# Kernel optimization log

Hardware: AMD Instinct MI355X
Metric: run time of the kernel (lower is better)

The kernel has to match this reference:

```python
import jax, jax.numpy as jnp
import numpy as np

DIM = 1024
NUM_HEADS = 16
HEAD_DIM = DIM // NUM_HEADS
EPS = 1e-5


def setup_inputs() -> dict:
    key = jax.random.key(0)
    ks = jax.random.split(key, 5)
    B, N = 2, 2048
    x = jax.random.normal(ks[0], (B, N, DIM), dtype=jnp.float32)
    # nn.Linear(dim, 3*dim): weight [3*dim, dim], bias [3*dim]
    w_qkv = jax.random.normal(ks[1], (3 * DIM, DIM), dtype=jnp.float32) * (DIM ** -0.5)
    b_qkv = jnp.zeros((3 * DIM,), dtype=jnp.float32)
    # qk-norm LayerNorm(head_dim) affine params
    q_gamma = jnp.ones((HEAD_DIM,), dtype=jnp.float32)
    q_beta = jnp.zeros((HEAD_DIM,), dtype=jnp.float32)
    k_gamma = jnp.ones((HEAD_DIM,), dtype=jnp.float32)
    k_beta = jnp.zeros((HEAD_DIM,), dtype=jnp.float32)
    # output projection nn.Linear(dim, dim)
    w_proj = jax.random.normal(ks[2], (DIM, DIM), dtype=jnp.float32) * (DIM ** -0.5)
    b_proj = jnp.zeros((DIM,), dtype=jnp.float32)
    return {
        "x": x,
        "w_qkv": w_qkv, "b_qkv": b_qkv,
        "q_gamma": q_gamma, "q_beta": q_beta,
        "k_gamma": k_gamma, "k_beta": k_beta,
        "w_proj": w_proj, "b_proj": b_proj,
    }


def _layernorm(t, gamma, beta):
    # LayerNorm over last dim (head_dim)
    mu = jnp.mean(t, axis=-1, keepdims=True)
    var = jnp.mean(jnp.square(t - mu), axis=-1, keepdims=True)
    return (t - mu) * jax.lax.rsqrt(var + EPS) * gamma + beta


def reference(x, w_qkv, b_qkv, q_gamma, q_beta, k_gamma, k_beta, w_proj, b_proj):
    B, N, C = x.shape
    H, D = NUM_HEADS, HEAD_DIM
    scale = D ** -0.5
    # QKV projection: [B,N,3C] -> [3,B,H,N,D]
    qkv = x @ w_qkv.T + b_qkv
    qkv = qkv.reshape(B, N, 3, H, D).transpose(2, 0, 3, 1, 4)
    q, k, v = qkv[0], qkv[1], qkv[2]
    # per-head qk-norm
    q = _layernorm(q, q_gamma, q_beta)
    k = _layernorm(k, k_gamma, k_beta)
    # scaled dot-product attention
    scores = jnp.einsum("bhqd,bhkd->bhqk", q, k) * scale
    attn = jax.nn.softmax(scores, axis=-1)
    out = jnp.einsum("bhqk,bhkd->bhqd", attn, v)  # [B,H,N,D]
    out = out.transpose(0, 2, 1, 3).reshape(B, N, C)
    # output projection
    return out @ w_proj.T + b_proj
```

## Files before the change

kernel.cpp:

```cpp
#include <hip/hip_runtime.h>

typedef _Float16 half8 __attribute__((ext_vector_type(8)));
typedef _Float16 half4 __attribute__((ext_vector_type(4)));
typedef float f32x4 __attribute__((ext_vector_type(4)));
typedef float f32x16 __attribute__((ext_vector_type(16)));
typedef unsigned int uint;
typedef uint uint2v __attribute__((ext_vector_type(2)));
typedef uint uint4v __attribute__((ext_vector_type(4)));

#define MFMA16(a, b, c) __builtin_amdgcn_mfma_f32_16x16x32_f16((a), (b), (c), 0, 0, 0)
#define MFMA32(a, b, c) __builtin_amdgcn_mfma_f32_32x32x16_f16((a), (b), (c), 0, 0, 0)

#define GLOAD16(g, l)                                            \
    __builtin_amdgcn_global_load_lds(                            \
        (const __attribute__((address_space(1))) void*)(g),      \
        (__attribute__((address_space(3))) void*)(l), 16, 0, 0)


__global__ __launch_bounds__(256) void cvt_all(const float* __restrict__ x,
                                               const float* __restrict__ wq,
                                               const float* __restrict__ wp,
                                               _Float16* __restrict__ xh,
                                               _Float16* __restrict__ wqh,
                                               _Float16* __restrict__ wph) {
    int i = blockIdx.x * 256 + threadIdx.x;
    const float* src;
    _Float16* dst;
    int off;
    if (i < 524288) { src = x; dst = xh; off = i; }
    else if (i < 917504) { src = wq; dst = wqh; off = i - 524288; }
    else { src = wp; dst = wph; off = i - 917504; }
    const float4* p = reinterpret_cast<const float4*>(src) + 2 * (size_t)off;
    float4 a = p[0], b = p[1];
    half8 o;
    o[0] = (_Float16)a.x; o[1] = (_Float16)a.y; o[2] = (_Float16)a.z; o[3] = (_Float16)a.w;
    o[4] = (_Float16)b.x; o[5] = (_Float16)b.y; o[6] = (_Float16)b.z; o[7] = (_Float16)b.w;
    reinterpret_cast<half8*>(dst)[off] = o;
}

template <int MT, int NT, int EPI>
__global__ __launch_bounds__(256) void gemm_nt(const _Float16* __restrict__ A,
                                               const _Float16* __restrict__ W,
                                               const float* __restrict__ bias,
                                               void* __restrict__ Cout, int K,
                                               const float* __restrict__ qg,
                                               const float* __restrict__ qb,
                                               const float* __restrict__ kg,
                                               const float* __restrict__ kb) {
    constexpr int TM = MT * 32;
    constexpr int TN = NT * 32;
    __shared__ __align__(16) _Float16 Al[2][TM * 64];
    __shared__ __align__(16) _Float16 Wl[2][TN * 64];
    const int tid = threadIdx.x, l = tid & 63, w = tid >> 6;
    const int lin = blockIdx.x + (blockIdx.y << 6);
    const int nwg = gridDim.x * gridDim.y;
    const int wg = (lin & 7) * (nwg >> 3) + (lin >> 3);
    const int bm = (wg & 63) * TM, bn = (wg >> 6) * TN;
    const int wr = (w >> 1) * (MT * 16), wc = (w & 1) * (NT * 16);
    const int srow = l >> 3;
    const int schunk = (l & 7) ^ srow;

    const _Float16* Ag = A + (size_t)(bm + (TM / 4) * w + srow) * K + 8 * schunk;
    const _Float16* Wg = W + (size_t)(bn + (TN / 4) * w + srow) * K + 8 * schunk;
    const int rswz = (l & 7) << 3;
    const int nk = K >> 6;

    auto stage = [&](int t, int buf) {
        const int kt = t << 6;
#pragma unroll
        for (int i = 0; i < MT; i++)
            GLOAD16(Ag + (size_t)(8 * i) * K + kt, &Al[buf][((TM / 4) * w + 8 * i) * 64]);
#pragma unroll
        for (int i = 0; i < NT; i++)
            GLOAD16(Wg + (size_t)(8 * i) * K + kt, &Wl[buf][((TN / 4) * w + 8 * i) * 64]);
    };

    f32x4 acc[MT][NT] = {};
    stage(0, 0);
    __syncthreads();
    for (int t = 0; t < nk; ++t) {
        const int cur = t & 1;
        if (t + 1 < nk) stage(t + 1, cur ^ 1);
#pragma unroll
        for (int ks = 0; ks < 2; ks++) {
            const int koff = (ks * 32 + (l >> 4) * 8) ^ rswz;
            half8 af[MT], wf[NT];
#pragma unroll
            for (int i = 0; i < MT; i++)
                af[i] = *(const half8*)&Al[cur][(wr + i * 16 + (l & 15)) * 64 + koff];
#pragma unroll
            for (int i = 0; i < NT; i++)
                wf[i] = *(const half8*)&Wl[cur][(wc + i * 16 + (l & 15)) * 64 + koff];
            __builtin_amdgcn_s_setprio(1);
#pragma unroll
            for (int mt = 0; mt < MT; mt++)
#pragma unroll
                for (int nt = 0; nt < NT; nt++)
                    acc[mt][nt] = MFMA16(af[mt], wf[nt], acc[mt][nt]);
            __builtin_amdgcn_s_setprio(0);
        }
        __syncthreads();
    }

    if (EPI == 0) {
        const int ncol = bn + wc;
        const int s = ncol >> 10;
        const int hh = (ncol >> 6) & 15;
        const float* gam = (s == 0) ? qg : kg;
        const float* bet = (s == 0) ? qb : kb;
        float ga[4], be[4];
        if (s < 2) {
#pragma unroll
            for (int nt = 0; nt < 4; nt++) {
                int d = nt * 16 + (l & 15);
                ga[nt] = gam[d];
                be[nt] = bet[d];
            }
        }
        const float cs = (s == 0) ? 0.18033688f : 1.f;
#pragma unroll
        for (int mt = 0; mt < MT; mt++)
#pragma unroll
            for (int r = 0; r < 4; r++) {
                float v[4];
                float sm = 0.f, s2 = 0.f;
#pragma unroll
                for (int nt = 0; nt < 4; nt++) {
                    v[nt] = acc[mt][nt][r] + bias[ncol + nt * 16 + (l & 15)];
                    sm += v[nt];
                    s2 += v[nt] * v[nt];
                }
                int m = bm + wr + mt * 16 + (l >> 4) * 4 + r;
                int b = m >> 11, nn = m & 2047;
                _Float16* dst = (_Float16*)Cout +
                    (size_t)((((s * 2 + b) * 16 + hh) * 2048 + nn) << 6);
                if (s < 2) {
#pragma unroll
                    for (int off = 1; off < 16; off <<= 1) {
                        sm += __shfl_xor(sm, off);
                        s2 += __shfl_xor(s2, off);
                    }
                    float mean = sm * (1.f / 64.f);
                    float var = s2 * (1.f / 64.f) - mean * mean;
                    float rs = rsqrtf(var + 1e-5f) * cs;
#pragma unroll
                    for (int nt = 0; nt < 4; nt++) {
                        int d = nt * 16 + (l & 15);
                        dst[d] = (_Float16)((v[nt] - mean) * rs * ga[nt] + be[nt] * cs);
                    }
                } else {
#pragma unroll
                    for (int nt = 0; nt < 4; nt++)
                        dst[nt * 16 + (l & 15)] = (_Float16)v[nt];
                }
            }
    } else {
#pragma unroll
        for (int mt = 0; mt < MT; mt++)
#pragma unroll
            for (int nt = 0; nt < NT; nt++)
#pragma unroll
                for (int r = 0; r < 4; r++) {
                    int m = bm + wr + mt * 16 + (l >> 4) * 4 + r;
                    int n = bn + wc + nt * 16 + (l & 15);
                    ((float*)Cout)[(size_t)m * 1024 + n] = acc[mt][nt][r] + bias[n];
                }
    }
}

template <int SPLIT>
__global__ __launch_bounds__(256, 4) void attn_kernel(const _Float16* __restrict__ qkv,
                                                      _Float16* __restrict__ out,
                                                      float* __restrict__ lpart) {
    const int tid = threadIdx.x;
    const int l = tid & 63, w = tid >> 6;
    const int l31 = l & 31, hi = l >> 5;
    const int bid = blockIdx.x;
    const int nwg = 512 * SPLIT;
    const int wg = (bid & 7) * (nwg >> 3) + (bid >> 3);
    int head, qt, quarter;
    if (SPLIT == 4) { head = wg >> 6; qt = (wg >> 2) & 15; quarter = wg & 3; }
    else            { head = wg >> 4; qt = wg & 15;        quarter = 0; }
    const int b = head >> 4, h = head & 15;
    const size_t hstride = (size_t)2048 * 64;
    const _Float16* Q = qkv + (size_t)((0 + b) * 16 + h) * hstride;
    const _Float16* Kp = qkv + (size_t)((2 + b) * 16 + h) * hstride + (size_t)quarter * 512 * 64;
    const _Float16* Vp = qkv + (size_t)((4 + b) * 16 + h) * hstride + (size_t)quarter * 512 * 64;
    const int NIT = (SPLIT == 4) ? 8 : 32;

    __shared__ __align__(16) _Float16 Kl[2][64 * 64];
    __shared__ __align__(16) _Float16 Vt[2][64 * 64];

    const int r0q = qt * 128 + w * 32;
    half8 qf[4];
    {
        const _Float16* Qrow = Q + (size_t)(r0q + l31) * 64 + 8 * hi;
#pragma unroll
        for (int dk = 0; dk < 4; dk++) qf[dk] = *(const half8*)&Qrow[16 * dk];
    }

    const int srow = l >> 3, sch = l & 7;
    auto stageK = [&](int it, _Float16* dst) {
#pragma unroll
        for (int t = 0; t < 2; t++) {
            int r0 = 16 * w + 8 * t;
            const _Float16* g = Kp + (size_t)(it * 64 + r0 + srow) * 64 + 8 * (sch ^ srow);
            GLOAD16(g, &dst[r0 * 64]);
        }
    };
    auto loadV = [&](int it, half8& v0, half8& v1) {
        const _Float16* g = Vp + (size_t)(it * 64 + 16 * w + srow) * 64 + 8 * sch;
        v0 = *(const half8*)g;
        v1 = *(const half8*)(g + 8 * 64);
    };
    auto scatterV = [&](half8 v0, half8 v1, _Float16* dst) {
        const int j0 = 16 * w + srow;
        const int d0 = 8 * sch;
#pragma unroll
        for (int i = 0; i < 8; i++) {
            const int sw = (i ^ sch) << 3;
            dst[(d0 + i) * 64 + (j0 ^ sw)] = v0[i];
            dst[(d0 + i) * 64 + ((j0 + 8) ^ sw)] = v1[i];
        }
    };

    float lrun = 0.f;
    f32x16 o0 = {}, o1 = {};

    half8 va, vb;
    stageK(0, Kl[0]);
    loadV(0, va, vb);
    scatterV(va, vb, Vt[0]);
    __syncthreads();

    const int kswz = (l31 & 7) << 3;
    const int vswz0 = ((l31 & 7) ^ (l31 >> 3)) << 3;
    const int vswz1 = vswz0 ^ (4 << 3);

    for (int it = 0; it < NIT; ++it) {
        const int cur = it & 1;
        const _Float16* Kc = Kl[cur];
        const _Float16* Vc = Vt[cur];
        if (it + 1 < NIT) {
            stageK(it + 1, Kl[cur ^ 1]);
            loadV(it + 1, va, vb);
        }

#pragma unroll
        for (int hf = 0; hf < 2; hf++) {
            f32x16 st = {};
#pragma unroll
            for (int dk = 0; dk < 4; dk++) {
                const int colr = 16 * dk + 8 * hi;
                half8 kf = *(const half8*)&Kc[(hf * 32 + l31) * 64 + (colr ^ kswz)];
                __builtin_amdgcn_s_setprio(1);
                st = MFMA32(kf, qf[dk], st);
                __builtin_amdgcn_s_setprio(0);
            }
#pragma unroll
            for (int r = 0; r < 16; r++) st[r] = exp2f(st[r]);
            lrun += (((st[0] + st[1]) + (st[2] + st[3])) +
                     ((st[4] + st[5]) + (st[6] + st[7]))) +
                    (((st[8] + st[9]) + (st[10] + st[11])) +
                     ((st[12] + st[13]) + (st[14] + st[15])));

#pragma unroll
            for (int cc = 0; cc < 2; cc++) {
                const int c = 2 * hf + cc;
                uint pk0 = __builtin_bit_cast(uint, __builtin_amdgcn_cvt_pkrtz(st[cc * 8 + 0], st[cc * 8 + 1]));
                uint pk1 = __builtin_bit_cast(uint, __builtin_amdgcn_cvt_pkrtz(st[cc * 8 + 2], st[cc * 8 + 3]));
                uint pk2 = __builtin_bit_cast(uint, __builtin_amdgcn_cvt_pkrtz(st[cc * 8 + 4], st[cc * 8 + 5]));
                uint pk3 = __builtin_bit_cast(uint, __builtin_amdgcn_cvt_pkrtz(st[cc * 8 + 6], st[cc * 8 + 7]));
                uint2v s02 = __builtin_amdgcn_permlane32_swap(pk0, pk2, false, false);
                uint2v s13 = __builtin_amdgcn_permlane32_swap(pk1, pk3, false, false);
                uint4v fu = {s02.x, s13.x, s02.y, s13.y};
                half8 pfrag = __builtin_bit_cast(half8, fu);
                const int colc = 16 * c + 8 * hi;
                half8 vf0 = *(const half8*)&Vc[l31 * 64 + (colc ^ vswz0)];
                half8 vf1 = *(const half8*)&Vc[(32 + l31) * 64 + (colc ^ vswz1)];
                __builtin_amdgcn_s_setprio(1);
                o0 = MFMA32(vf0, pfrag, o0);
                o1 = MFMA32(vf1, pfrag, o1);
                __builtin_amdgcn_s_setprio(0);
            }
        }

        if (it + 1 < NIT) scatterV(va, vb, Vt[cur ^ 1]);
        __syncthreads();
    }

    lrun += __shfl_xor(lrun, 32);
    const int tok = r0q + l31;
    if (SPLIT == 4) {
        _Float16* orow = out + (size_t)quarter * 4194304 + (size_t)(b * 2048 + tok) * 1024 + h * 64;
#pragma unroll
        for (int g = 0; g < 4; g++) {
            half4 h4a, h4b;
#pragma unroll
            for (int j = 0; j < 4; j++) {
                h4a[j] = (_Float16)o0[4 * g + j];
                h4b[j] = (_Float16)o1[4 * g + j];
            }
            *(half4*)&orow[8 * g + 4 * hi] = h4a;
            *(half4*)&orow[32 + 8 * g + 4 * hi] = h4b;
        }
        if (!hi) lpart[quarter * 65536 + (b * 16 + h) * 2048 + tok] = lrun;
    } else {
        const float inv = __builtin_amdgcn_rcpf(lrun);
        _Float16* orow = out + (size_t)(b * 2048 + tok) * 1024 + h * 64;
#pragma unroll
        for (int g = 0; g < 4; g++) {
            half4 h4a, h4b;
#pragma unroll
            for (int j = 0; j < 4; j++) {
                h4a[j] = (_Float16)(o0[4 * g + j] * inv);
                h4b[j] = (_Float16)(o1[4 * g + j] * inv);
            }
            *(half4*)&orow[8 * g + 4 * hi] = h4a;
            *(half4*)&orow[32 + 8 * g + 4 * hi] = h4b;
        }
    }
}

__global__ __launch_bounds__(256) void merge_attn(const _Float16* __restrict__ onum,
                                                  const float* __restrict__ lpart,
                                                  _Float16* __restrict__ attnh) {
    const int i = blockIdx.x * 256 + threadIdx.x;
    const int tokb = i >> 7;
    const int c0 = (i & 127) * 8;
    const int h = c0 >> 6;
    const int bb = tokb >> 11, tok = tokb & 2047;
    const int li = (bb * 16 + h) * 2048 + tok;
    float lt = lpart[li] + lpart[65536 + li] + lpart[131072 + li] + lpart[196608 + li];
    float inv = __builtin_amdgcn_rcpf(lt);
    float acc[8] = {};
#pragma unroll
    for (int q = 0; q < 4; q++) {
        half8 v = *(const half8*)&onum[(size_t)q * 4194304 + (size_t)tokb * 1024 + c0];
#pragma unroll
        for (int j = 0; j < 8; j++) acc[j] += (float)v[j];
    }
    half8 o;
#pragma unroll
    for (int j = 0; j < 8; j++) o[j] = (_Float16)(acc[j] * inv);
    *(half8*)&attnh[(size_t)tokb * 1024 + c0] = o;
}

extern "C" void kernel_launch(void* const* d_in, const int* in_sizes, int n_in,
                              void* d_out, int out_size, void* d_ws, size_t ws_size,
                              hipStream_t stream) {
    const float* x = (const float*)d_in[0];
    const float* w_qkv = (const float*)d_in[1];
    const float* b_qkv = (const float*)d_in[2];
    const float* q_gamma = (const float*)d_in[3];
    const float* q_beta = (const float*)d_in[4];
    const float* k_gamma = (const float*)d_in[5];
    const float* k_beta = (const float*)d_in[6];
    const float* w_proj = (const float*)d_in[7];
    const float* b_proj = (const float*)d_in[8];

    char* ws = (char*)d_ws;
    _Float16* xh = (_Float16*)(ws + 0);
    _Float16* wqkvh = (_Float16*)(ws + 8388608);
    _Float16* wprojh = (_Float16*)(ws + 14680064);
    _Float16* qkvh = (_Float16*)(ws + 16777216);
    _Float16* attnh = (_Float16*)(ws + 41943040);
    _Float16* onum = (_Float16*)(ws + 50331648);
    float* lp = (float*)(ws + 83886080);
    const bool split = ws_size >= 84934656;

    cvt_all<<<4096, 256, 0, stream>>>(x, w_qkv, w_proj, xh, wqkvh, wprojh);

    gemm_nt<2, 4, 0><<<dim3(64, 24), 256, 0, stream>>>(xh, wqkvh, b_qkv, (void*)qkvh, 1024,
                                                       q_gamma, q_beta, k_gamma, k_beta);

    if (split) {
        attn_kernel<4><<<2048, 256, 0, stream>>>(qkvh, onum, lp);
        merge_attn<<<2048, 256, 0, stream>>>(onum, lp, attnh);
    } else {
        attn_kernel<1><<<512, 256, 0, stream>>>(qkvh, attnh, nullptr);
    }

    gemm_nt<2, 2, 1><<<dim3(64, 16), 256, 0, stream>>>(attnh, wprojh, b_proj, d_out, 1024,
                                                       nullptr, nullptr, nullptr, nullptr);
}
```

Baseline: 224.8 us.

## Add 256x256-tile 8-phase pipelined QKV GEMM and defer V load in attention

Replaces the QKV projection GEMM with a new 512-thread kernel that uses 256x256 output tiles. It splits each K step into eight phases that interleave global-to-LDS staging with MFMA work, separated by barriers and explicit vmcnt waits, and keeps the fused qk-layernorm epilogue. The attention kernel now loads V from global and scatters it in one step after the compute loop, instead of prefetching into registers, which cuts register pressure but exposes more load latency. The projection GEMM drops its unused layernorm epilogue. The larger tile gives only 192 workgroups, which may underfill the device.

```diff
diff --git a/kernel.cpp b/kernel.cpp
--- a/kernel.cpp
+++ b/kernel.cpp
@@ -38,15 +38,139 @@
     reinterpret_cast<half8*>(dst)[off] = o;
 }
 
-template <int MT, int NT, int EPI>
+__global__ __launch_bounds__(512) void gemm1_8ph(const _Float16* __restrict__ A,
+                                                 const _Float16* __restrict__ W,
+                                                 const float* __restrict__ bias,
+                                                 _Float16* __restrict__ qkv,
+                                                 const float* __restrict__ qg,
+                                                 const float* __restrict__ qb,
+                                                 const float* __restrict__ kg,
+                                                 const float* __restrict__ kb) {
+    constexpr int K = 1024;
+    __shared__ __align__(16) _Float16 AL[2][2][2][64][64];
+    __shared__ __align__(16) _Float16 BL[2][2][2][64][64];
+    const int tid = threadIdx.x, l = tid & 63, w = tid >> 6;
+    const int wm = w >> 2, wn = w & 3;
+    const int lin = blockIdx.x + (blockIdx.y << 4);
+    const int wg = (lin & 7) * 24 + (lin >> 3);
+    const int bm = (wg & 15) * 256, bn = (wg >> 4) * 256;
+    const int srow = l >> 3, sch = (l & 7) ^ (srow & 7);
+    const int rowA = l & 15;
+
+    auto stageA = [&](int t, int h) {
+        const int buf = t & 1;
+#pragma unroll
+        for (int r = 0; r < 2; r++) {
+            int absrow = r * 128 + h * 64 + w * 8 + srow;
+            GLOAD16(A + (size_t)(bm + absrow) * K + t * 64 + 8 * sch, &AL[buf][h][r][w * 8][0]);
+        }
+    };
+    auto stageB = [&](int t, int h) {
+        const int buf = t & 1;
+#pragma unroll
+        for (int r = 0; r < 2; r++) {
+            int absrow = h * 128 + r * 64 + w * 8 + srow;
+            GLOAD16(W + (size_t)(bn + absrow) * K + t * 64 + 8 * sch, &BL[buf][h][r][w * 8][0]);
+        }
+    };
+
+    f32x4 acc[8][4] = {};
+
+    stageA(0, 0); stageA(0, 1); stageB(0, 0); stageB(0, 1); stageA(1, 0);
+    asm volatile("s_waitcnt vmcnt(2)" ::: "memory");
+    __builtin_amdgcn_s_barrier();
+
+#define PH(BUF, QM, QK, STAGE, VM)                                                        \
+    {                                                                                     \
+        half8 af[4], wf[4];                                                               \
+        const int kc = (((QK) * 4 + (l >> 4)) ^ (l & 7)) * 8;                             \
+        _Pragma("unroll") for (int f = 0; f < 4; f++)                                     \
+            af[f] = *(const half8*)&AL[BUF][QM][wm][f * 16 + rowA][kc];                   \
+        _Pragma("unroll") for (int f = 0; f < 4; f++)                                     \
+            wf[f] = *(const half8*)&BL[BUF][wn >> 1][wn & 1][f * 16 + rowA][kc];          \
+        STAGE;                                                                            \
+        __builtin_amdgcn_s_barrier();                                                     \
+        asm volatile("s_waitcnt lgkmcnt(0)" ::: "memory");                                \
+        __builtin_amdgcn_sched_barrier(0);                                                \
+        __builtin_amdgcn_s_setprio(1);                                                    \
+        _Pragma("unroll") for (int mf = 0; mf < 4; mf++)                                  \
+            _Pragma("unroll") for (int nf = 0; nf < 4; nf++)                              \
+                acc[(QM) * 4 + mf][nf] = MFMA16(af[mf], wf[nf], acc[(QM) * 4 + mf][nf]);  \
+        __builtin_amdgcn_s_setprio(0);                                                    \
+        if (VM) asm volatile("s_waitcnt vmcnt(2)" ::: "memory");                          \
+        __builtin_amdgcn_s_barrier();                                                     \
+    }
+
+    for (int i = 0; i < 8; ++i) {
+        const int t1 = 2 * i + 1;
+        const int s2 = (i < 7) ? 2 * i + 2 : 14;
+        const int s3 = (i < 7) ? 2 * i + 3 : 15;
+        PH(0, 0, 0, stageA(t1, 1), 0)
+        PH(0, 1, 0, stageB(t1, 0), 0)
+        PH(0, 0, 1, stageB(t1, 1), 0)
+        PH(0, 1, 1, stageA(s2, 0), 1)
+        PH(1, 0, 0, stageA(s2, 1), 0)
+        PH(1, 1, 0, stageB(s2, 0), 0)
+        PH(1, 0, 1, stageB(s2, 1), 0)
+        PH(1, 1, 1, stageA(s3, 0), 1)
+    }
+#undef PH
+
+    const int ncol = bn + wn * 64;
+    const int s = ncol >> 10;
+    const int hh = (ncol >> 6) & 15;
+    const float* gam = (s == 0) ? qg : kg;
+    const float* bet = (s == 0) ? qb : kb;
+    float ga[4], be[4];
+    if (s < 2) {
+#pragma unroll
+        for (int nf = 0; nf < 4; nf++) {
+            int d = nf * 16 + rowA;
+            ga[nf] = gam[d];
+            be[nf] = bet[d];
+        }
+    }
+    const float cs = (s == 0) ? 0.18033688f : 1.f;
+#pragma unroll
+    for (int mfa = 0; mfa < 8; mfa++)
+#pragma unroll
+        for (int r = 0; r < 4; r++) {
+            float v[4];
+            float sm = 0.f, s2s = 0.f;
+#pragma unroll
+            for (int nf = 0; nf < 4; nf++) {
+                v[nf] = acc[mfa][nf][r] + bias[ncol + nf * 16 + rowA];
+                sm += v[nf];
+                s2s += v[nf] * v[nf];
+            }
+            int m = bm + wm * 128 + mfa * 16 + (l >> 4) * 4 + r;
+            int b = m >> 11, nn = m & 2047;
+            _Float16* dst = qkv + (size_t)((((s * 2 + b) * 16 + hh) * 2048 + nn) << 6);
+            if (s < 2) {
+#pragma unroll
+                for (int off = 1; off < 16; off <<= 1) {
+                    sm += __shfl_xor(sm, off);
+                    s2s += __shfl_xor(s2s, off);
+                }
+                float mean = sm * (1.f / 64.f);
+                float var = s2s * (1.f / 64.f) - mean * mean;
+                float rs = rsqrtf(var + 1e-5f) * cs;
+#pragma unroll
+                for (int nf = 0; nf < 4; nf++)
+                    dst[nf * 16 + rowA] = (_Float16)((v[nf] - mean) * rs * ga[nf] + be[nf] * cs);
+            } else {
+#pragma unroll
+                for (int nf = 0; nf < 4; nf++)
+                    dst[nf * 16 + rowA] = (_Float16)v[nf];
+            }
+        }
+}
+
+template <int MT, int NT>
 __global__ __launch_bounds__(256) void gemm_nt(const _Float16* __restrict__ A,
                                                const _Float16* __restrict__ W,
                                                const float* __restrict__ bias,
-                                               void* __restrict__ Cout, int K,
-                                               const float* __restrict__ qg,
-                                               const float* __restrict__ qb,
-                                               const float* __restrict__ kg,
-                                               const float* __restrict__ kb) {
+                                               float* __restrict__ Cout, int K) {
     constexpr int TM = MT * 32;
     constexpr int TN = NT * 32;
     __shared__ __align__(16) _Float16 Al[2][TM * 64];
@@ -101,71 +225,16 @@
         }
         __syncthreads();
     }
-
-    if (EPI == 0) {
-        const int ncol = bn + wc;
-        const int s = ncol >> 10;
-        const int hh = (ncol >> 6) & 15;
-        const float* gam = (s == 0) ? qg : kg;
-        const float* bet = (s == 0) ? qb : kb;
-        float ga[4], be[4];
-        if (s < 2) {
-#pragma unroll
-            for (int nt = 0; nt < 4; nt++) {
-                int d = nt * 16 + (l & 15);
-                ga[nt] = gam[d];
-                be[nt] = bet[d];
-            }
-        }
-        const float cs = (s == 0) ? 0.18033688f : 1.f;
-#pragma unroll
-        for (int mt = 0; mt < MT; mt++)
+#pragma unroll
+    for (int mt = 0; mt < MT; mt++)
+#pragma unroll
+        for (int nt = 0; nt < NT; nt++)
 #pragma unroll
             for (int r = 0; r < 4; r++) {
-                float v[4];
-                float sm = 0.f, s2 = 0.f;
-#pragma unroll
-                for (int nt = 0; nt < 4; nt++) {
-                    v[nt] = acc[mt][nt][r] + bias[ncol + nt * 16 + (l & 15)];
-                    sm += v[nt];
-                    s2 += v[nt] * v[nt];
-                }
                 int m = bm + wr + mt * 16 + (l >> 4) * 4 + r;
-                int b = m >> 11, nn = m & 2047;
-                _Float16* dst = (_Float16*)Cout +
-                    (size_t)((((s * 2 + b) * 16 + hh) * 2048 + nn) << 6);
-                if (s < 2) {
-#pragma unroll
-                    for (int off = 1; off < 16; off <<= 1) {
-                        sm += __shfl_xor(sm, off);
-                        s2 += __shfl_xor(s2, off);
-                    }
-                    float mean = sm * (1.f / 64.f);
-                    float var = s2 * (1.f / 64.f) - mean * mean;
-                    float rs = rsqrtf(var + 1e-5f) * cs;
-#pragma unroll
-                    for (int nt = 0; nt < 4; nt++) {
-                        int d = nt * 16 + (l & 15);
-                        dst[d] = (_Float16)((v[nt] - mean) * rs * ga[nt] + be[nt] * cs);
-                    }
-                } else {
-#pragma unroll
-                    for (int nt = 0; nt < 4; nt++)
-                        dst[nt * 16 + (l & 15)] = (_Float16)v[nt];
-                }
-            }
-    } else {
-#pragma unroll
-        for (int mt = 0; mt < MT; mt++)
-#pragma unroll
-            for (int nt = 0; nt < NT; nt++)
-#pragma unroll
-                for (int r = 0; r < 4; r++) {
-                    int m = bm + wr + mt * 16 + (l >> 4) * 4 + r;
-                    int n = bn + wc + nt * 16 + (l & 15);
-                    ((float*)Cout)[(size_t)m * 1024 + n] = acc[mt][nt][r] + bias[n];
-                }
-    }
+                int n = bn + wc + nt * 16 + (l & 15);
+                Cout[(size_t)m * 1024 + n] = acc[mt][nt][r] + bias[n];
+            }
 }
 
 template <int SPLIT>
@@ -208,12 +277,10 @@
             GLOAD16(g, &dst[r0 * 64]);
         }
     };
-    auto loadV = [&](int it, half8& v0, half8& v1) {
+    auto loadScatterV = [&](int it, _Float16* dst) {
         const _Float16* g = Vp + (size_t)(it * 64 + 16 * w + srow) * 64 + 8 * sch;
-        v0 = *(const half8*)g;
-        v1 = *(const half8*)(g + 8 * 64);
-    };
-    auto scatterV = [&](half8 v0, half8 v1, _Float16* dst) {
+        half8 v0 = *(const half8*)g;
+        half8 v1 = *(const half8*)(g + 8 * 64);
         const int j0 = 16 * w + srow;
         const int d0 = 8 * sch;
 #pragma unroll
@@ -227,10 +294,8 @@
     float lrun = 0.f;
     f32x16 o0 = {}, o1 = {};
 
-    half8 va, vb;
     stageK(0, Kl[0]);
-    loadV(0, va, vb);
-    scatterV(va, vb, Vt[0]);
+    loadScatterV(0, Vt[0]);
     __syncthreads();
 
     const int kswz = (l31 & 7) << 3;
@@ -241,10 +306,7 @@
         const int cur = it & 1;
         const _Float16* Kc = Kl[cur];
         const _Float16* Vc = Vt[cur];
-        if (it + 1 < NIT) {
-            stageK(it + 1, Kl[cur ^ 1]);
-            loadV(it + 1, va, vb);
-        }
+        if (it + 1 < NIT) stageK(it + 1, Kl[cur ^ 1]);
 
 #pragma unroll
         for (int hf = 0; hf < 2; hf++) {
@@ -285,7 +347,7 @@
             }
         }
 
-        if (it + 1 < NIT) scatterV(va, vb, Vt[cur ^ 1]);
+        if (it + 1 < NIT) loadScatterV(it + 1, Vt[cur ^ 1]);
         __syncthreads();
     }
 
@@ -371,8 +433,8 @@
 
     cvt_all<<<4096, 256, 0, stream>>>(x, w_qkv, w_proj, xh, wqkvh, wprojh);
 
-    gemm_nt<2, 4, 0><<<dim3(64, 24), 256, 0, stream>>>(xh, wqkvh, b_qkv, (void*)qkvh, 1024,
-                                                       q_gamma, q_beta, k_gamma, k_beta);
+    gemm1_8ph<<<dim3(16, 12), 512, 0, stream>>>(xh, wqkvh, b_qkv, qkvh,
+                                                q_gamma, q_beta, k_gamma, k_beta);
 
     if (split) {
         attn_kernel<4><<<2048, 256, 0, stream>>>(qkvh, onum, lp);
@@ -381,6 +443,5 @@
         attn_kernel<1><<<512, 256, 0, stream>>>(qkvh, attnh, nullptr);
     }
 
-    gemm_nt<2, 2, 1><<<dim3(64, 16), 256, 0, stream>>>(attnh, wprojh, b_proj, d_out, 1024,
-                                                       nullptr, nullptr, nullptr, nullptr);
-}
+    gemm_nt<2, 2><<<dim3(64, 16), 256, 0, stream>>>(attnh, wprojh, b_proj, (float*)d_out, 1024);
+}
```

After: 222.9 us. Within noise of the previous version (-0.9%).
